# Kernel optimization log

Hardware: AMD Instinct MI355X
Metric: run time of the kernel (lower is better)

Reference implementation:

```python
import jax, jax.numpy as jnp
import numpy as np

E = 1024   # embedding_size
K = 64     # key_size
DH = 64    # head_size
H = 16     # layer_size (num heads)
F = 4096   # hidden_size
B, S = 4, 2048
EPS = float(np.finfo(np.float32).eps)  # torch RMSNorm default eps


def setup_inputs() -> dict:
    key = jax.random.key(0)
    ks = jax.random.split(key, 12)
    embeddings = jax.random.normal(ks[0], (B, S, E), dtype=jnp.float32)
    # causal additive mask: 0 on/below diagonal, -1e9 above
    tri = jnp.triu(jnp.ones((S, S), dtype=bool), k=1)
    causal_buffer = jnp.where(tri, -1e9, 0.0).astype(jnp.float32)[None]  # [1,S,S]
    # standard RoPE cos/sin buffers over the key dim
    inv_freq = 1.0 / (10000.0 ** (jnp.arange(0, K // 2, dtype=jnp.float32) * 2.0 / K))
    ang = jnp.arange(S, dtype=jnp.float32)[:, None] * inv_freq[None, :]  # [S,K/2]
    ang = jnp.concatenate([ang, ang], axis=-1)                           # [S,K]
    cos_buffer = jnp.cos(ang)[None]  # [1,S,K]
    sin_buffer = jnp.sin(ang)[None]
    sc = 0.02
    wq = jax.random.normal(ks[1], (H, E, K), dtype=jnp.float32) * sc
    wk = jax.random.normal(ks[2], (H, E, K), dtype=jnp.float32) * sc
    wv = jax.random.normal(ks[3], (H, E, DH), dtype=jnp.float32) * sc
    w_proj = jax.random.normal(ks[4], (E, E), dtype=jnp.float32) * sc
    attn_norm_w = jnp.ones((E,), dtype=jnp.float32)
    mlp_norm_w = jnp.ones((E,), dtype=jnp.float32)
    w_up = jax.random.normal(ks[5], (E, F), dtype=jnp.float32) * sc
    w_gate = jax.random.normal(ks[6], (E, F), dtype=jnp.float32) * sc
    w_down = jax.random.normal(ks[7], (F, E), dtype=jnp.float32) * sc
    return {"embeddings": embeddings, "causal_buffer": causal_buffer,
            "cos_buffer": cos_buffer, "sin_buffer": sin_buffer,
            "wq": wq, "wk": wk, "wv": wv, "w_proj": w_proj,
            "attn_norm_w": attn_norm_w, "mlp_norm_w": mlp_norm_w,
            "w_up": w_up, "w_gate": w_gate, "w_down": w_down}


def _rmsnorm(x, w):
    ms = jnp.mean(x * x, axis=-1, keepdims=True)
    return x * jax.lax.rsqrt(ms + EPS) * w


def _rotate(x, cos, sin):
    # x: [B,H,S,K]; cos/sin: [1,1,S,K]. swapped = cat(second_half, first_half)
    swapped = jnp.concatenate([x[..., K // 2:], x[..., :K // 2]], axis=-1)
    return cos * x + sin * swapped


def reference(embeddings, causal_buffer, cos_buffer, sin_buffer,
              wq, wk, wv, w_proj, attn_norm_w, mlp_norm_w,
              w_up, w_gate, w_down):
    cos = cos_buffer[:, None]  # [1,1,S,K]
    sin = sin_buffer[:, None]
    # NOTE: original computes attention_norm(embeddings) but feeds RAW
    # embeddings to the heads; we reproduce that faithfully.
    q = _rotate(jnp.einsum('bse,hek->bhsk', embeddings, wq), cos, sin)
    k = _rotate(jnp.einsum('bse,hek->bhsk', embeddings, wk), cos, sin)
    v = jnp.einsum('bse,hed->bhsd', embeddings, wv)
    scores = jnp.einsum('bhsk,bhtk->bhst', q, k) / jnp.sqrt(jnp.float32(K))
    scores = scores + causal_buffer[:, None]  # broadcast over heads
    weights = jax.nn.softmax(scores, axis=-1)
    attn = jnp.einsum('bhst,bhtd->bhsd', weights, v)  # [B,H,S,DH]
    attn = attn.transpose(0, 2, 1, 3).reshape(attn.shape[0], attn.shape[2], H * DH)
    x = embeddings + attn @ w_proj
    h = _rmsnorm(x, mlp_norm_w)
    mlp = (h @ w_up) * jax.nn.elu(h @ w_gate)
    return x + mlp @ w_down
```

## Files before the change

kernel.cpp:

```cpp
#include <hip/hip_runtime.h>
#include <cstdint>
#include <cstddef>

#define E_DIM 1024
#define S_LEN 2048
#define NB 4
#define NH 16
#define F_DIM 4096

typedef __attribute__((ext_vector_type(8))) __bf16 bf16x8;
typedef __attribute__((ext_vector_type(4))) __bf16 bf16x4;
typedef __attribute__((ext_vector_type(4))) float f32x4;
typedef __attribute__((ext_vector_type(16))) float f32x16;

__device__ __forceinline__ f32x4 mfma16(bf16x8 a, bf16x8 b, f32x4 c) {
  return __builtin_amdgcn_mfma_f32_16x16x32_bf16(a, b, c, 0, 0, 0);
}
__device__ __forceinline__ f32x16 mfma32(bf16x8 a, bf16x8 b, f32x16 c) {
  return __builtin_amdgcn_mfma_f32_32x32x16_bf16(a, b, c, 0, 0, 0);
}

__device__ __forceinline__ unsigned short f2bf(float f) {
  __bf16 h = (__bf16)f;
  return __builtin_bit_cast(unsigned short, h);
}

__device__ __forceinline__ void gl_lds16(const void* gptr, void* lptr) {
  __builtin_amdgcn_global_load_lds(
      (const __attribute__((address_space(1))) void*)gptr,
      (__attribute__((address_space(3))) void*)lptr, 16, 0, 0);
}


__global__ __launch_bounds__(256) void cast_emb_kernel(
    const float4* __restrict__ in, ushort4* __restrict__ out) {
  int i = blockIdx.x * 256 + threadIdx.x;
  float4 v = in[i];
  ushort4 o;
  o.x = f2bf(v.x); o.y = f2bf(v.y); o.z = f2bf(v.z); o.w = f2bf(v.w);
  out[i] = o;
}

__global__ __launch_bounds__(256) void transpose_cast_kernel(
    const float* __restrict__ in, unsigned short* __restrict__ out, int R, int C) {
  __shared__ float tile[32][33];
  const int bz = blockIdx.z;
  const float* ip = in + (size_t)bz * R * C;
  const int r0 = blockIdx.y * 32, c0 = blockIdx.x * 32;
  const int tc = threadIdx.x & 31, tr = threadIdx.x >> 5;
#pragma unroll
  for (int i = 0; i < 4; ++i)
    tile[tr + i * 8][tc] = ip[(size_t)(r0 + tr + i * 8) * C + (c0 + tc)];
  __syncthreads();
#pragma unroll
  for (int i = 0; i < 4; ++i)
    out[(size_t)(bz * C + c0 + tr + i * 8) * R + (r0 + tc)] = f2bf(tile[tc][tr + i * 8]);
}

__global__ __launch_bounds__(256) void transpose_cast_qkv(
    const float* __restrict__ wq, const float* __restrict__ wk,
    const float* __restrict__ wv, unsigned short* __restrict__ out) {
  __shared__ float tile[32][33];
  const int bz = blockIdx.z;
  const int which = bz >> 4, hz = bz & 15;
  const float* ip =
      (which == 0 ? wq : which == 1 ? wk : wv) + (size_t)hz * 1024 * 64;
  unsigned short* op = out + (size_t)which * 1024 * 1024;
  const int r0 = blockIdx.y * 32, c0 = blockIdx.x * 32;
  const int tc = threadIdx.x & 31, tr = threadIdx.x >> 5;
#pragma unroll
  for (int i = 0; i < 4; ++i)
    tile[tr + i * 8][tc] = ip[(size_t)(r0 + tr + i * 8) * 64 + (c0 + tc)];
  __syncthreads();
#pragma unroll
  for (int i = 0; i < 4; ++i)
    op[(size_t)(hz * 64 + c0 + tr + i * 8) * 1024 + (r0 + tc)] =
        f2bf(tile[tc][tr + i * 8]);
}

__global__ __launch_bounds__(256) void transpose_cast_upgate(
    const float* __restrict__ wup, const float* __restrict__ wgate,
    unsigned short* __restrict__ out) {
  __shared__ float tile[32][33];
  const int z = blockIdx.z & 1;
  const float* ip = z ? wgate : wup;
  const int r0 = blockIdx.y * 32, c0 = blockIdx.x * 32;
  const int tc = threadIdx.x & 31, tr = threadIdx.x >> 5;
#pragma unroll
  for (int i = 0; i < 4; ++i)
    tile[tr + i * 8][tc] = ip[(size_t)(r0 + tr + i * 8) * F_DIM + (c0 + tc)];
  __syncthreads();
#pragma unroll
  for (int i = 0; i < 4; ++i) {
    const int c = c0 + tr + i * 8;
    const int row = 64 * (c >> 5) + (c & 31) + z * 32;
    out[(size_t)row * E_DIM + (r0 + tc)] = f2bf(tile[tc][tr + i * 8]);
  }
}

template <int EPI, int KD>
__global__ __launch_bounds__(256) void gemm_bt(
    const unsigned short* __restrict__ A, const unsigned short* __restrict__ Bt,
    const float* __restrict__ aux, const float* __restrict__ cosb,
    const float* __restrict__ sinb,
    unsigned short* __restrict__ qout, unsigned short* __restrict__ kout,
    unsigned short* __restrict__ vtout, float* __restrict__ fout,
    unsigned short* __restrict__ gout) {
  __shared__ unsigned short As[128 * 64];
  __shared__ unsigned short Bs[128 * 64];
  const int t = threadIdx.x;
  const int lane = t & 63, w = t >> 6;
  const int l31 = lane & 31, half = lane >> 5;
  const int wm = (w >> 1) * 64, wn = (w & 1) * 64;
  const int m0 = blockIdx.y * 128, n0 = blockIdx.x * 128;
  const int sr = t >> 3, sc = t & 7;
  const int gcoff = (sc ^ (sr & 7)) * 8;
  const unsigned short* ga = A + (size_t)(m0 + sr) * KD + gcoff;
  const unsigned short* gb = Bt + (size_t)(n0 + sr) * KD + gcoff;
  unsigned short* lA = &As[sr * 64 + sc * 8];
  unsigned short* lB = &Bs[sr * 64 + sc * 8];
  const int xh = lane & 7;
  f32x16 acc[2][2] = {};
  for (int k0 = 0; k0 < KD; k0 += 64) {
    __syncthreads();
#pragma unroll
    for (int i = 0; i < 4; ++i) {
      gl_lds16(ga + (size_t)(i * 32) * KD + k0, lA + i * 32 * 64);
      gl_lds16(gb + (size_t)(i * 32) * KD + k0, lB + i * 32 * 64);
    }
    __syncthreads();
#pragma unroll
    for (int ksl = 0; ksl < 4; ++ksl) {
      const int cp = ((ksl * 2 + half) ^ xh) * 8;
      bf16x8 af[2], bfr[2];
#pragma unroll
      for (int mi = 0; mi < 2; ++mi)
        af[mi] = *reinterpret_cast<const bf16x8*>(&As[(wm + mi * 32 + l31) * 64 + cp]);
#pragma unroll
      for (int ni = 0; ni < 2; ++ni)
        bfr[ni] = *reinterpret_cast<const bf16x8*>(&Bs[(wn + ni * 32 + l31) * 64 + cp]);
#pragma unroll
      for (int mi = 0; mi < 2; ++mi)
#pragma unroll
        for (int ni = 0; ni < 2; ++ni)
          acc[mi][ni] = mfma32(af[mi], bfr[ni], acc[mi][ni]);
    }
  }
  if (EPI == 0) {
#pragma unroll
    for (int mi = 0; mi < 2; ++mi)
#pragma unroll
      for (int ni = 0; ni < 2; ++ni) {
        const int n = n0 + wn + ni * 32 + l31;
        const int seg = n >> 10, rest = n & 1023, hh = rest >> 6, kk = rest & 63;
#pragma unroll
        for (int reg = 0; reg < 16; ++reg) {
          const int m = m0 + wm + mi * 32 + (reg & 3) + 8 * (reg >> 2) + 4 * half;
          const int b = m >> 11, s = m & 2047;
          const float v = acc[mi][ni][reg];
          if (seg == 2) {
            vtout[(((size_t)(b * NH + hh)) * 64 + kk) * S_LEN + s] = f2bf(v);
          } else {
            const float sw = acc[mi][ni ^ 1][reg];
            const float cv = cosb[s * 64 + kk], sv = sinb[s * 64 + kk];
            const float scl = (seg == 0) ? 0.125f : 1.0f;
            unsigned short* dst = (seg == 0) ? qout : kout;
            dst[(((size_t)(b * NH + hh)) * S_LEN + s) * 64 + kk] =
                f2bf((cv * v + sv * sw) * scl);
          }
        }
      }
  } else if (EPI == 3) {
    const int col = ((n0 + wn) >> 1) + l31;
#pragma unroll
    for (int mi = 0; mi < 2; ++mi)
#pragma unroll
      for (int reg = 0; reg < 16; ++reg) {
        const int m = m0 + wm + mi * 32 + (reg & 3) + 8 * (reg >> 2) + 4 * half;
        const float u = acc[mi][0][reg], gt = acc[mi][1][reg];
        const float e = gt > 0.f ? gt : (__expf(gt) - 1.f);
        gout[(size_t)m * F_DIM + col] = f2bf(u * e);
      }
  } else {
#pragma unroll
    for (int mi = 0; mi < 2; ++mi)
#pragma unroll
      for (int ni = 0; ni < 2; ++ni) {
        const int n = n0 + wn + ni * 32 + l31;
#pragma unroll
        for (int reg = 0; reg < 16; ++reg) {
          const int m = m0 + wm + mi * 32 + (reg & 3) + 8 * (reg >> 2) + 4 * half;
          const size_t idx = (size_t)m * 1024 + n;
          fout[idx] = aux[idx] + acc[mi][ni][reg];
        }
      }
  }
}

#define PS_STRIDE 68
__global__ __launch_bounds__(256) void flash_attn(
    const unsigned short* __restrict__ qb, const unsigned short* __restrict__ kb,
    const unsigned short* __restrict__ vtb, unsigned short* __restrict__ attn) {
  __shared__ unsigned short Ks[64 * 64];
  __shared__ unsigned short Vts[64 * 64];
  __shared__ unsigned short Ps[128 * PS_STRIDE];
  const int t = threadIdx.x, lane = t & 63, w = t >> 6;
  const int quad = lane >> 4, l15 = lane & 15;
  const int qt = 15 - blockIdx.y;
  const int bh = blockIdx.x;
  const int b = bh >> 4, hh = bh & 15;
  const unsigned short* qg = qb + (size_t)bh * S_LEN * 64;
  const unsigned short* kg = kb + (size_t)bh * S_LEN * 64;
  const unsigned short* vg = vtb + (size_t)bh * 64 * S_LEN;
  bf16x8 aq[2][2];
#pragma unroll
  for (int mi = 0; mi < 2; ++mi)
#pragma unroll
    for (int ks = 0; ks < 2; ++ks)
      aq[mi][ks] = *reinterpret_cast<const bf16x8*>(
          qg + (size_t)(qt * 128 + w * 32 + mi * 16 + l15) * 64 + ks * 32 + quad * 8);
  f32x4 o[2][4] = {};
  float lpart[2][4] = {};
  const int srk = t >> 3, sck = t & 7;
  const int gck = ((sck ^ (srk & 7)) * 8);
  const int xh = l15 & 7;
  const int ktmax = 2 * qt + 1;
  for (int kt = 0; kt <= ktmax; ++kt) {
    __syncthreads();
#pragma unroll
    for (int i = 0; i < 2; ++i) {
      gl_lds16(kg + (size_t)(kt * 64 + srk + i * 32) * 64 + gck,
               &Ks[(srk + i * 32) * 64 + sck * 8]);
      gl_lds16(vg + (size_t)(srk + i * 32) * S_LEN + kt * 64 + gck,
               &Vts[(srk + i * 32) * 64 + sck * 8]);
    }
    __syncthreads();
    f32x4 sacc[2][4];
#pragma unroll
    for (int mi = 0; mi < 2; ++mi)
#pragma unroll
      for (int nt = 0; nt < 4; ++nt) sacc[mi][nt] = (f32x4){-8.f, -8.f, -8.f, -8.f};
#pragma unroll
    for (int nt = 0; nt < 4; ++nt) {
      bf16x8 b0 = *reinterpret_cast<const bf16x8*>(
          &Ks[(nt * 16 + l15) * 64 + ((quad ^ xh) * 8)]);
      bf16x8 b1 = *reinterpret_cast<const bf16x8*>(
          &Ks[(nt * 16 + l15) * 64 + (((4 + quad) ^ xh) * 8)]);
#pragma unroll
      for (int mi = 0; mi < 2; ++mi) {
        sacc[mi][nt] = mfma16(aq[mi][0], b0, sacc[mi][nt]);
        sacc[mi][nt] = mfma16(aq[mi][1], b1, sacc[mi][nt]);
      }
    }
    if (kt >= 2 * qt) {
#pragma unroll
      for (int mi = 0; mi < 2; ++mi)
#pragma unroll
        for (int nt = 0; nt < 4; ++nt)
#pragma unroll
          for (int rg = 0; rg < 4; ++rg) {
            const int row = qt * 128 + w * 32 + mi * 16 + quad * 4 + rg;
            const int col = kt * 64 + nt * 16 + l15;
            if (col > row) sacc[mi][nt][rg] = -1e9f;
          }
    }
#pragma unroll
    for (int mi = 0; mi < 2; ++mi)
#pragma unroll
      for (int nt = 0; nt < 4; ++nt)
#pragma unroll
        for (int rg = 0; rg < 4; ++rg) {
          const float p = __expf(sacc[mi][nt][rg]);
          lpart[mi][rg] += p;
          Ps[(w * 32 + mi * 16 + quad * 4 + rg) * PS_STRIDE + nt * 16 + l15] = f2bf(p);
        }
#pragma unroll
    for (int ks = 0; ks < 2; ++ks) {
      bf16x8 ap[2];
#pragma unroll
      for (int mi = 0; mi < 2; ++mi) {
        const unsigned short* pp =
            &Ps[(w * 32 + mi * 16 + l15) * PS_STRIDE + ks * 32 + quad * 8];
        bf16x4 lo = *reinterpret_cast<const bf16x4*>(pp);
        bf16x4 hi = *reinterpret_cast<const bf16x4*>(pp + 4);
        ap[mi] = __builtin_shufflevector(lo, hi, 0, 1, 2, 3, 4, 5, 6, 7);
      }
#pragma unroll
      for (int vt = 0; vt < 4; ++vt) {
        bf16x8 bv = *reinterpret_cast<const bf16x8*>(
            &Vts[(vt * 16 + l15) * 64 + (((ks * 4 + quad) ^ xh) * 8)]);
#pragma unroll
        for (int mi = 0; mi < 2; ++mi) o[mi][vt] = mfma16(ap[mi], bv, o[mi][vt]);
      }
    }
  }
  float linv[2][4];
#pragma unroll
  for (int mi = 0; mi < 2; ++mi)
#pragma unroll
    for (int rg = 0; rg < 4; ++rg) {
      float rs = lpart[mi][rg];
#pragma unroll
      for (int d = 1; d < 16; d <<= 1) rs += __shfl_xor(rs, d);
      linv[mi][rg] = 1.0f / rs;
    }
#pragma unroll
  for (int mi = 0; mi < 2; ++mi)
#pragma unroll
    for (int vt = 0; vt < 4; ++vt)
#pragma unroll
      for (int rg = 0; rg < 4; ++rg) {
        const int row = w * 32 + mi * 16 + quad * 4 + rg;
        const int s = qt * 128 + row;
        const float ov = o[mi][vt][rg] * linv[mi][rg];
        attn[((size_t)(b * S_LEN + s)) * E_DIM + hh * 64 + vt * 16 + l15] = f2bf(ov);
      }
}

__global__ __launch_bounds__(256) void rmsnorm_kernel(
    const float* __restrict__ x, const float* __restrict__ wgt,
    unsigned short* __restrict__ hout) {
  const int row = blockIdx.x;
  const int t = threadIdx.x;
  const float4 v = reinterpret_cast<const float4*>(x + (size_t)row * E_DIM)[t];
  float ss = v.x * v.x + v.y * v.y + v.z * v.z + v.w * v.w;
#pragma unroll
  for (int d = 1; d < 64; d <<= 1) ss += __shfl_xor(ss, d);
  __shared__ float red[4];
  if ((t & 63) == 0) red[t >> 6] = ss;
  __syncthreads();
  const float tot = red[0] + red[1] + red[2] + red[3];
  const float sc = rsqrtf(tot * (1.f / 1024.f) + 1.1920929e-07f);
  const float4 g = reinterpret_cast<const float4*>(wgt)[t];
  ushort4 ov;
  ov.x = f2bf(v.x * sc * g.x);
  ov.y = f2bf(v.y * sc * g.y);
  ov.z = f2bf(v.z * sc * g.z);
  ov.w = f2bf(v.w * sc * g.w);
  reinterpret_cast<ushort4*>(hout + (size_t)row * E_DIM)[t] = ov;
}

extern "C" void kernel_launch(void* const* d_in, const int* in_sizes, int n_in,
                              void* d_out, int out_size, void* d_ws, size_t ws_size,
                              hipStream_t stream) {
  (void)in_sizes; (void)n_in; (void)out_size; (void)ws_size;
  const float* emb = (const float*)d_in[0];
  const float* cosb = (const float*)d_in[2];
  const float* sinb = (const float*)d_in[3];
  const float* wq = (const float*)d_in[4];
  const float* wk = (const float*)d_in[5];
  const float* wv = (const float*)d_in[6];
  const float* wproj = (const float*)d_in[7];
  const float* mlpw = (const float*)d_in[9];
  const float* wup = (const float*)d_in[10];
  const float* wgate = (const float*)d_in[11];
  const float* wdown = (const float*)d_in[12];
  float* out = (float*)d_out;
  char* ws = (char*)d_ws;
  unsigned short* wqkv_t = (unsigned short*)(ws + 0);
  unsigned short* wproj_t = (unsigned short*)(ws + 6291456);
  unsigned short* wupgate_t = (unsigned short*)(ws + 8388608);
  unsigned short* wdown_t = (unsigned short*)(ws + 25165824);
  unsigned short* embb = (unsigned short*)(ws + 33554432);
  unsigned short* qbuf = (unsigned short*)(ws + 50331648);
  unsigned short* kbuf = (unsigned short*)(ws + 67108864);
  unsigned short* vtbuf = (unsigned short*)(ws + 83886080);
  unsigned short* gbuf = (unsigned short*)(ws + 33554432);
  unsigned short* attnb = (unsigned short*)(ws + 100663296);
  float* xbuf = (float*)(ws + 117440512);
  unsigned short* hbuf = (unsigned short*)(ws + 150994944);

  dim3 blk(256);
  cast_emb_kernel<<<8192, blk, 0, stream>>>((const float4*)emb, (ushort4*)embb);
  transpose_cast_qkv<<<dim3(2, 32, 48), blk, 0, stream>>>(wq, wk, wv, wqkv_t);
  transpose_cast_kernel<<<dim3(32, 32, 1), blk, 0, stream>>>(wproj, wproj_t, 1024, 1024);
  transpose_cast_upgate<<<dim3(128, 32, 2), blk, 0, stream>>>(wup, wgate, wupgate_t);
  transpose_cast_kernel<<<dim3(32, 128, 1), blk, 0, stream>>>(wdown, wdown_t, 4096, 1024);
  gemm_bt<0, 1024><<<dim3(24, 64), blk, 0, stream>>>(
      embb, wqkv_t, nullptr, cosb, sinb, qbuf, kbuf, vtbuf, nullptr, nullptr);
  flash_attn<<<dim3(64, 16), blk, 0, stream>>>(qbuf, kbuf, vtbuf, attnb);
  gemm_bt<1, 1024><<<dim3(8, 64), blk, 0, stream>>>(
      attnb, wproj_t, emb, nullptr, nullptr, nullptr, nullptr, nullptr, xbuf, nullptr);
  rmsnorm_kernel<<<8192, blk, 0, stream>>>(xbuf, mlpw, hbuf);
  gemm_bt<3, 1024><<<dim3(64, 64), blk, 0, stream>>>(
      hbuf, wupgate_t, nullptr, nullptr, nullptr, nullptr, nullptr, nullptr, nullptr, gbuf);
  gemm_bt<2, 4096><<<dim3(8, 64), blk, 0, stream>>>(
      gbuf, wdown_t, xbuf, nullptr, nullptr, nullptr, nullptr, nullptr, out, nullptr);
}
```

Baseline: 634.6 us.

## Replace up/gate GEMM with 256x256-tile 512-thread pipelined kernel

Adds a dedicated up/gate projection GEMM that uses 256x256 output tiles, 512 threads and double-buffered direct global-to-LDS loads. Loads are issued in half-K stages interleaved with 16x16x32 MFMA blocks, using explicit vmcnt waits, barriers and setprio. The ELU-gated product is computed in the epilogue. Larger tiles are meant to raise arithmetic intensity and overlap loads with MFMA work on the largest GEMM. The cost is heavy register and LDS use, which limits occupancy, and a fragile hand-written wait schedule.

```diff
diff --git a/kernel.cpp b/kernel.cpp
--- a/kernel.cpp
+++ b/kernel.cpp
@@ -170,17 +170,6 @@
           }
         }
       }
-  } else if (EPI == 3) {
-    const int col = ((n0 + wn) >> 1) + l31;
-#pragma unroll
-    for (int mi = 0; mi < 2; ++mi)
-#pragma unroll
-      for (int reg = 0; reg < 16; ++reg) {
-        const int m = m0 + wm + mi * 32 + (reg & 3) + 8 * (reg >> 2) + 4 * half;
-        const float u = acc[mi][0][reg], gt = acc[mi][1][reg];
-        const float e = gt > 0.f ? gt : (__expf(gt) - 1.f);
-        gout[(size_t)m * F_DIM + col] = f2bf(u * e);
-      }
   } else {
 #pragma unroll
     for (int mi = 0; mi < 2; ++mi)
@@ -195,6 +184,166 @@
         }
       }
   }
+}
+
+#define VMW6() asm volatile("s_waitcnt vmcnt(6)" ::: "memory")
+#define FENCE() asm volatile("" ::: "memory")
+#define BARX()                        \
+  do {                                \
+    FENCE();                          \
+    __builtin_amdgcn_s_barrier();     \
+    FENCE();                          \
+  } while (0)
+
+__global__ __launch_bounds__(512, 2) void gemm256_upgate(
+    const unsigned short* __restrict__ A, const unsigned short* __restrict__ Bt,
+    unsigned short* __restrict__ gout) {
+  constexpr int KD = 1024;
+  constexpr int NT = KD / 64;
+  __shared__ unsigned short As[2 * 16384];
+  __shared__ unsigned short Bs[2 * 16384];
+  const int tid = threadIdx.x;
+  const int lane = tid & 63, w = tid >> 6;
+  const int l15 = lane & 15, quad = (lane >> 4) & 3;
+  const int wm = (w >> 2) * 128, wn = (w & 3) * 64;
+  const int m0 = blockIdx.y * 256, n0 = blockIdx.x * 256;
+  const int r = tid >> 2;
+  const int csrc = ((tid & 3) ^ (r & 3)) * 8;
+  const unsigned short* gA = A + (size_t)(m0 + r) * KD + csrc;
+  const unsigned short* gB = Bt + (size_t)(n0 + r) * KD + csrc;
+  const int ldst = tid * 8;
+  const int xk = (quad ^ (l15 & 3)) * 8;
+  const int abase = (wm + l15) * 32 + xk;
+  const int bbase = (wn + l15) * 32 + xk;
+
+#define STG_A(bufi, s, tt)                                                     \
+  do {                                                                         \
+    gl_lds16(gA + (size_t)(tt) * 64 + (s) * 32,                                \
+             &As[(bufi) * 16384 + (s) * 8192 + ldst]);                         \
+    gl_lds16(gA + (size_t)(tt) * 64 + (s) * 32 + (size_t)128 * KD,             \
+             &As[(bufi) * 16384 + (s) * 8192 + 4096 + ldst]);                  \
+  } while (0)
+#define STG_B(bufi, s, tt)                                                     \
+  do {                                                                         \
+    gl_lds16(gB + (size_t)(tt) * 64 + (s) * 32,                                \
+             &Bs[(bufi) * 16384 + (s) * 8192 + ldst]);                         \
+    gl_lds16(gB + (size_t)(tt) * 64 + (s) * 32 + (size_t)128 * KD,             \
+             &Bs[(bufi) * 16384 + (s) * 8192 + 4096 + ldst]);                  \
+  } while (0)
+
+  f32x4 acc[8][4] = {};
+  bf16x8 b0[4], b1[4], a[4];
+
+#define MFMA_BLK(mb, bfr)                                                      \
+  do {                                                                         \
+    __builtin_amdgcn_s_setprio(1);                                             \
+    _Pragma("unroll") for (int mi = 0; mi < 4; ++mi)                           \
+        _Pragma("unroll") for (int ni = 0; ni < 4; ++ni)                       \
+            acc[(mb) + mi][ni] = mfma16(a[mi], bfr[ni], acc[(mb) + mi][ni]);   \
+    __builtin_amdgcn_s_setprio(0);                                             \
+  } while (0)
+
+  STG_B(0, 0, 0); FENCE();
+  STG_A(0, 0, 0); FENCE();
+  STG_B(0, 1, 0); FENCE();
+  STG_A(0, 1, 0); FENCE();
+  VMW6();
+  BARX();
+#pragma unroll
+  for (int ni = 0; ni < 4; ++ni)
+    b0[ni] = *reinterpret_cast<const bf16x8*>(&Bs[ni * 512 + bbase]);
+  STG_B(1, 0, 1);
+
+  int buf = 0;
+  for (int t = 0; t < NT - 1; ++t, buf ^= 1) {
+    const int nx = buf ^ 1;
+    VMW6();
+    BARX();
+#pragma unroll
+    for (int mi = 0; mi < 4; ++mi)
+      a[mi] = *reinterpret_cast<const bf16x8*>(&As[buf * 16384 + mi * 512 + abase]);
+    STG_A(nx, 0, t + 1);
+    MFMA_BLK(0, b0);
+    VMW6();
+    BARX();
+#pragma unroll
+    for (int mi = 0; mi < 4; ++mi)
+      a[mi] = *reinterpret_cast<const bf16x8*>(
+          &As[buf * 16384 + (4 + mi) * 512 + abase]);
+#pragma unroll
+    for (int ni = 0; ni < 4; ++ni)
+      b1[ni] = *reinterpret_cast<const bf16x8*>(
+          &Bs[buf * 16384 + 8192 + ni * 512 + bbase]);
+    STG_B(nx, 1, t + 1);
+    MFMA_BLK(4, b0);
+    VMW6();
+    BARX();
+#pragma unroll
+    for (int mi = 0; mi < 4; ++mi)
+      a[mi] = *reinterpret_cast<const bf16x8*>(
+          &As[buf * 16384 + 8192 + mi * 512 + abase]);
+    STG_A(nx, 1, t + 1);
+    MFMA_BLK(0, b1);
+    VMW6();
+    BARX();
+#pragma unroll
+    for (int mi = 0; mi < 4; ++mi)
+      a[mi] = *reinterpret_cast<const bf16x8*>(
+          &As[buf * 16384 + 8192 + (4 + mi) * 512 + abase]);
+#pragma unroll
+    for (int ni = 0; ni < 4; ++ni)
+      b0[ni] = *reinterpret_cast<const bf16x8*>(
+          &Bs[nx * 16384 + ni * 512 + bbase]);
+    if (t + 2 < NT) STG_B(buf, 0, t + 2);
+    MFMA_BLK(4, b1);
+  }
+  {
+    asm volatile("s_waitcnt vmcnt(4)" ::: "memory");
+    BARX();
+#pragma unroll
+    for (int mi = 0; mi < 4; ++mi)
+      a[mi] = *reinterpret_cast<const bf16x8*>(&As[buf * 16384 + mi * 512 + abase]);
+    MFMA_BLK(0, b0);
+    asm volatile("s_waitcnt vmcnt(2)" ::: "memory");
+    BARX();
+#pragma unroll
+    for (int mi = 0; mi < 4; ++mi)
+      a[mi] = *reinterpret_cast<const bf16x8*>(
+          &As[buf * 16384 + (4 + mi) * 512 + abase]);
+#pragma unroll
+    for (int ni = 0; ni < 4; ++ni)
+      b1[ni] = *reinterpret_cast<const bf16x8*>(
+          &Bs[buf * 16384 + 8192 + ni * 512 + bbase]);
+    MFMA_BLK(4, b0);
+    asm volatile("s_waitcnt vmcnt(0)" ::: "memory");
+    BARX();
+#pragma unroll
+    for (int mi = 0; mi < 4; ++mi)
+      a[mi] = *reinterpret_cast<const bf16x8*>(
+          &As[buf * 16384 + 8192 + mi * 512 + abase]);
+    MFMA_BLK(0, b1);
+#pragma unroll
+    for (int mi = 0; mi < 4; ++mi)
+      a[mi] = *reinterpret_cast<const bf16x8*>(
+          &As[buf * 16384 + 8192 + (4 + mi) * 512 + abase]);
+    MFMA_BLK(4, b1);
+  }
+  const int colb = ((n0 + wn) >> 1) + l15;
+  const int mrow = m0 + wm + quad * 4;
+#pragma unroll
+  for (int mi = 0; mi < 8; ++mi)
+#pragma unroll
+    for (int np = 0; np < 2; ++np)
+#pragma unroll
+      for (int rg = 0; rg < 4; ++rg) {
+        const float uu = acc[mi][np][rg], gg = acc[mi][np + 2][rg];
+        const float e = gg > 0.f ? gg : (__expf(gg) - 1.f);
+        gout[(size_t)(mrow + mi * 16 + rg) * F_DIM + colb + np * 16] =
+            f2bf(uu * e);
+      }
+#undef STG_A
+#undef STG_B
+#undef MFMA_BLK
 }
 
 #define PS_STRIDE 68
@@ -382,8 +531,7 @@
   gemm_bt<1, 1024><<<dim3(8, 64), blk, 0, stream>>>(
       attnb, wproj_t, emb, nullptr, nullptr, nullptr, nullptr, nullptr, xbuf, nullptr);
   rmsnorm_kernel<<<8192, blk, 0, stream>>>(xbuf, mlpw, hbuf);
-  gemm_bt<3, 1024><<<dim3(64, 64), blk, 0, stream>>>(
-      hbuf, wupgate_t, nullptr, nullptr, nullptr, nullptr, nullptr, nullptr, nullptr, gbuf);
+  gemm256_upgate<<<dim3(32, 32), dim3(512), 0, stream>>>(hbuf, wupgate_t, gbuf);
   gemm_bt<2, 4096><<<dim3(8, 64), blk, 0, stream>>>(
       gbuf, wdown_t, xbuf, nullptr, nullptr, nullptr, nullptr, nullptr, out, nullptr);
 }
```

Measured after the change: 621.0 us. 1.02x faster.

## Replace up/gate GEMM with 256x256-tile, 512-thread pipelined kernel

Applied to the files above, without the earlier changes.

Adds a dedicated up/gate GEMM kernel that uses 256x256 output tiles with 8 waves per block, an XOR-swizzled double-buffered LDS stage fed by direct global-to-LDS loads, and explicit vmcnt waits and barriers interleaved with MFMA groups at raised wave priority. The ELU-gated epilogue moves into this kernel, and the old EPI==3 path is removed. The larger tile is meant to raise arithmetic intensity and overlap loads with compute in the largest GEMM. In exchange it uses a big LDS footprint and hand-tuned wait counts that are fragile.

```diff
diff --git a/kernel.cpp b/kernel.cpp
--- a/kernel.cpp
+++ b/kernel.cpp
@@ -170,17 +170,6 @@
           }
         }
       }
-  } else if (EPI == 3) {
-    const int col = ((n0 + wn) >> 1) + l31;
-#pragma unroll
-    for (int mi = 0; mi < 2; ++mi)
-#pragma unroll
-      for (int reg = 0; reg < 16; ++reg) {
-        const int m = m0 + wm + mi * 32 + (reg & 3) + 8 * (reg >> 2) + 4 * half;
-        const float u = acc[mi][0][reg], gt = acc[mi][1][reg];
-        const float e = gt > 0.f ? gt : (__expf(gt) - 1.f);
-        gout[(size_t)m * F_DIM + col] = f2bf(u * e);
-      }
   } else {
 #pragma unroll
     for (int mi = 0; mi < 2; ++mi)
@@ -195,6 +184,112 @@
         }
       }
   }
+}
+
+#define FENCE() asm volatile("" ::: "memory")
+#define BARX()                        \
+  do {                                \
+    FENCE();                          \
+    __builtin_amdgcn_s_barrier();     \
+    FENCE();                          \
+  } while (0)
+
+__global__ __launch_bounds__(512, 2) void gemm256_upgate(
+    const unsigned short* __restrict__ A, const unsigned short* __restrict__ Bt,
+    unsigned short* __restrict__ gout) {
+  constexpr int KD = 1024;
+  constexpr int NT = KD / 64;
+  __shared__ unsigned short L[8 * 8192];
+  const int tid = threadIdx.x;
+  const int lane = tid & 63, w = tid >> 6;
+  const int l31 = lane & 31, half = lane >> 5;
+  const int wm = (w >> 2) * 128, wn = (w & 3) * 64;
+  const int m0 = blockIdx.y * 256, n0 = blockIdx.x * 256;
+  const int r = tid >> 2;
+  const int csrc = ((tid & 3) ^ ((r ^ (r >> 2)) & 3)) * 8;
+  const unsigned short* gA = A + (size_t)(m0 + r) * KD + csrc;
+  const unsigned short* gB = Bt + (size_t)(n0 + r) * KD + csrc;
+  const int ldst = tid * 8;
+  const int sA = (l31 ^ (l31 >> 2)) & 3;
+
+  f32x16 acc[4][2] = {};
+  bf16x8 a[4], b[2];
+
+#define STG(ridx, gp, koff)                                                    \
+  do {                                                                         \
+    gl_lds16((gp) + (koff), &L[(ridx) * 8192 + ldst]);                         \
+    gl_lds16((gp) + (koff) + (size_t)128 * KD,                                 \
+             &L[(ridx) * 8192 + 4096 + ldst]);                                 \
+  } while (0)
+
+#define RD(hh, kl, bufi)                                                       \
+  do {                                                                         \
+    const int xo = ((((kl) * 2 + half) ^ sA)) * 8;                             \
+    const int ra = ((bufi) * 4 + 1 + 2 * (hh)) * 8192;                         \
+    const int rb = ((bufi) * 4 + 2 * (hh)) * 8192;                             \
+    _Pragma("unroll") for (int mi = 0; mi < 4; ++mi)                           \
+        a[mi] = *reinterpret_cast<const bf16x8*>(                              \
+            &L[ra + (wm + mi * 32 + l31) * 32 + xo]);                          \
+    _Pragma("unroll") for (int ni = 0; ni < 2; ++ni)                           \
+        b[ni] = *reinterpret_cast<const bf16x8*>(                              \
+            &L[rb + (wn + ni * 32 + l31) * 32 + xo]);                          \
+  } while (0)
+
+#define MFMA8()                                                                \
+  do {                                                                         \
+    __builtin_amdgcn_s_setprio(1);                                             \
+    _Pragma("unroll") for (int mi = 0; mi < 4; ++mi)                           \
+        _Pragma("unroll") for (int ni = 0; ni < 2; ++ni)                       \
+            acc[mi][ni] = mfma32(a[mi], b[ni], acc[mi][ni]);                   \
+    __builtin_amdgcn_s_setprio(0);                                             \
+  } while (0)
+
+  STG(0, gB, 0); FENCE();
+  STG(1, gA, 0); FENCE();
+  STG(2, gB, 32); FENCE();
+  STG(3, gA, 32); FENCE();
+
+  int buf = 0;
+  for (int t = 0; t < NT; ++t, buf ^= 1) {
+    const int nx = buf ^ 1;
+    const bool pre = (t + 1 < NT);
+    const int ko = (t + 1) * 64;
+    asm volatile("s_waitcnt vmcnt(4)" ::: "memory");
+    BARX();
+    RD(0, 0, buf);
+    if (pre) STG(nx * 4 + 0, gB, ko);
+    MFMA8();
+    BARX();
+    RD(0, 1, buf);
+    if (pre) STG(nx * 4 + 1, gA, ko);
+    MFMA8();
+    if (pre) {
+      asm volatile("s_waitcnt vmcnt(4)" ::: "memory");
+    } else {
+      asm volatile("s_waitcnt vmcnt(0)" ::: "memory");
+    }
+    BARX();
+    RD(1, 0, buf);
+    if (pre) STG(nx * 4 + 2, gB, ko + 32);
+    MFMA8();
+    BARX();
+    RD(1, 1, buf);
+    if (pre) STG(nx * 4 + 3, gA, ko + 32);
+    MFMA8();
+  }
+  const int colb = ((n0 + wn) >> 1) + l31;
+#pragma unroll
+  for (int mi = 0; mi < 4; ++mi)
+#pragma unroll
+    for (int reg = 0; reg < 16; ++reg) {
+      const int m = m0 + wm + mi * 32 + (reg & 3) + 8 * (reg >> 2) + 4 * half;
+      const float uu = acc[mi][0][reg], gg = acc[mi][1][reg];
+      const float e = gg > 0.f ? gg : (__expf(gg) - 1.f);
+      gout[(size_t)m * F_DIM + colb] = f2bf(uu * e);
+    }
+#undef STG
+#undef RD
+#undef MFMA8
 }
 
 #define PS_STRIDE 68
@@ -382,8 +477,7 @@
   gemm_bt<1, 1024><<<dim3(8, 64), blk, 0, stream>>>(
       attnb, wproj_t, emb, nullptr, nullptr, nullptr, nullptr, nullptr, xbuf, nullptr);
   rmsnorm_kernel<<<8192, blk, 0, stream>>>(xbuf, mlpw, hbuf);
-  gemm_bt<3, 1024><<<dim3(64, 64), blk, 0, stream>>>(
-      hbuf, wupgate_t, nullptr, nullptr, nullptr, nullptr, nullptr, nullptr, nullptr, gbuf);
+  gemm256_upgate<<<dim3(32, 32), dim3(512), 0, stream>>>(hbuf, wupgate_t, gbuf);
   gemm_bt<2, 4096><<<dim3(8, 64), blk, 0, stream>>>(
       gbuf, wdown_t, xbuf, nullptr, nullptr, nullptr, nullptr, nullptr, out, nullptr);
 }
```

Measured after the change: 634.5 us. Within noise of the previous version (-0.0%).
